# Kernel optimization log

Hardware: AMD Instinct MI355X
Metric: run time of the kernel (lower is better)

The kernel has to match this reference:

```python
import jax, jax.numpy as jnp
import numpy as np

DRUG_DIM, PROT_DIM, HIDDEN_DIM, OUTPUT_DIM = 128, 128, 256, 256


def setup_inputs() -> dict:
    key = jax.random.key(0)
    ks = jax.random.split(key, 7)
    B, n_d, n_p = 8, 64, 1024
    s = lambda d: 1.0 / np.sqrt(d)
    return {
        "X_d": jax.random.normal(ks[0], (B, n_d, DRUG_DIM), dtype=jnp.float32),
        "X_p": jax.random.normal(ks[1], (B, n_p, PROT_DIM), dtype=jnp.float32),
        # nn.Linear(in, out) weights have shape (out, in); we store transposed (in, out)
        "W_d": jax.random.uniform(ks[2], (DRUG_DIM, HIDDEN_DIM), jnp.float32, -s(DRUG_DIM), s(DRUG_DIM)),
        "W_p": jax.random.uniform(ks[3], (PROT_DIM, HIDDEN_DIM), jnp.float32, -s(PROT_DIM), s(PROT_DIM)),
        "W_a": jax.random.uniform(ks[4], (DRUG_DIM, OUTPUT_DIM), jnp.float32, -s(DRUG_DIM), s(DRUG_DIM)),
        "W_b": jax.random.uniform(ks[5], (PROT_DIM, OUTPUT_DIM), jnp.float32, -s(PROT_DIM), s(PROT_DIM)),
        "w_score": jax.random.uniform(ks[6], (HIDDEN_DIM,), jnp.float32, -s(HIDDEN_DIM), s(HIDDEN_DIM)),
    }


def reference(X_d, X_p, W_d, W_p, W_a, W_b, w_score):
    # Projections: (B, n_d, H), (B, n_p, H), (B, n_d, O), (B, n_p, O)
    hd = jnp.einsum("bik,kh->bih", X_d, W_d)
    hp = jnp.einsum("bjk,kh->bjh", X_p, W_p)
    fd = jnp.einsum("bik,ko->bio", X_d, W_a)
    fp = jnp.einsum("bjk,ko->bjo", X_p, W_b)

    # N_ij = tanh(hd_i + hp_j): (B, n_d, n_p, H); scores = N @ w_score
    N = jnp.tanh(hd[:, :, None, :] + hp[:, None, :, :])
    scores = jnp.einsum("bijh,h->bij", N, w_score)
    A = jax.nn.softmax(scores, axis=-1)  # softmax over protein dim

    # f_ij = tanh(fd_i + fp_j): (B, n_d, n_p, O)
    f = jnp.tanh(fd[:, :, None, :] + fp[:, None, :, :])
    X_int = jnp.einsum("bij,bijo->bo", A, f)  # sum over i and j
    return X_int
```

## Files before the change

### kernel.cpp

```cpp
#include <hip/hip_runtime.h>

#define NB   8
#define ND   64
#define NP   1024
#define KDIM 128
#define HID  256
#define OUTD 256
#define CSC  2.885390081777927f

typedef __attribute__((ext_vector_type(8))) short  bf16x8;
typedef __attribute__((ext_vector_type(4))) float  f32x4;


__device__ __forceinline__ ushort f2bf(float f) {
    unsigned u = __float_as_uint(f);
    return (ushort)((u + 0x7FFFu + ((u >> 16) & 1u)) >> 16);
}

__global__ __launch_bounds__(256) void k_cast(
    const float* __restrict__ Xd, const float* __restrict__ Xp,
    const float* __restrict__ Wd, const float* __restrict__ Wa,
    const float* __restrict__ Wp, const float* __restrict__ Wb,
    ushort* __restrict__ Xdbf, ushort* __restrict__ Xpbf,
    ushort* __restrict__ WdT, ushort* __restrict__ WaT,
    ushort* __restrict__ WpT, ushort* __restrict__ WbT) {
    int blk = blockIdx.x, t = threadIdx.x;
    if (blk < 1024) {
        size_t i = ((size_t)blk << 10) + ((size_t)t << 2);
        float4 v = *(const float4*)(Xp + i);
        ushort4 o; o.x = f2bf(v.x); o.y = f2bf(v.y); o.z = f2bf(v.z); o.w = f2bf(v.w);
        *(ushort4*)(Xpbf + i) = o;
    } else if (blk < 1088) {
        size_t i = ((size_t)(blk - 1024) << 10) + ((size_t)t << 2);
        float4 v = *(const float4*)(Xd + i);
        ushort4 o; o.x = f2bf(v.x); o.y = f2bf(v.y); o.z = f2bf(v.z); o.w = f2bf(v.w);
        *(ushort4*)(Xdbf + i) = o;
    } else {
        int r = blk - 1088, mat = r >> 5;
        const float* W = (mat == 0) ? Wd : (mat == 1) ? Wa : (mat == 2) ? Wp : Wb;
        ushort* WT = (mat == 0) ? WdT : (mat == 1) ? WaT : (mat == 2) ? WpT : WbT;
        int o0 = ((r & 31) << 10) + (t << 2);
        int n = o0 >> 7, k0 = o0 & 127;
        ushort4 o;
        o.x = f2bf(W[(k0 + 0) * HID + n]);
        o.y = f2bf(W[(k0 + 1) * HID + n]);
        o.z = f2bf(W[(k0 + 2) * HID + n]);
        o.w = f2bf(W[(k0 + 3) * HID + n]);
        *(ushort4*)(WT + o0) = o;
    }
}

__global__ __launch_bounds__(256) void k_proj_mfma(
    const ushort* __restrict__ Xpbf, const ushort* __restrict__ Xdbf,
    const ushort* __restrict__ WdT, const ushort* __restrict__ WaT,
    const ushort* __restrict__ WpT, const ushort* __restrict__ WbT,
    float* __restrict__ Ehd, float* __restrict__ Efd,
    float* __restrict__ EhpT, float* __restrict__ Efp) {
    int blk = blockIdx.x, t = threadIdx.x;
    const ushort *A, *B;
    float* out; size_t obase; int ostride, am0, bn0;
    if (blk < 512) {
        int mt = blk >> 2, nt = blk & 3;
        A = Xpbf; am0 = mt * 64; B = WbT; bn0 = nt * 64;
        out = Efp; obase = (size_t)am0 * HID + bn0; ostride = HID;
    } else if (blk < 1024) {
        int r = blk - 512, b = r >> 6, rr = r & 63;
        int mt = rr >> 4, nt = rr & 15;
        A = WpT; am0 = mt * 64;
        B = Xpbf + (size_t)b * NP * KDIM; bn0 = nt * 64;
        out = EhpT; obase = ((size_t)(b * 256 + am0)) * NP + bn0; ostride = NP;
    } else if (blk < 1056) {
        int r = blk - 1024; int mt = r >> 2, nt = r & 3;
        A = Xdbf; am0 = mt * 64; B = WdT; bn0 = nt * 64;
        out = Ehd; obase = (size_t)am0 * HID + bn0; ostride = HID;
    } else {
        int r = blk - 1056; int mt = r >> 2, nt = r & 3;
        A = Xdbf; am0 = mt * 64; B = WaT; bn0 = nt * 64;
        out = Efd; obase = (size_t)am0 * HID + bn0; ostride = HID;
    }
    int l = t & 63, w = t >> 6;
    int wm = (w >> 1) << 5, wn = (w & 1) << 5;
    int lr = l & 15, lk = (l >> 4) << 3;
    const ushort* Ab = A + (size_t)(am0 + wm + lr) * KDIM + lk;
    const ushort* Bb = B + (size_t)(bn0 + wn + lr) * KDIM + lk;

    bf16x8 af[2][4], bfr[2][4];
#pragma unroll
    for (int f = 0; f < 2; ++f)
#pragma unroll
        for (int ks = 0; ks < 4; ++ks) {
            af[f][ks]  = *(const bf16x8*)(Ab + (size_t)(f << 4) * KDIM + (ks << 5));
            bfr[f][ks] = *(const bf16x8*)(Bb + (size_t)(f << 4) * KDIM + (ks << 5));
        }

    f32x4 acc[2][2];
#pragma unroll
    for (int mf = 0; mf < 2; ++mf)
#pragma unroll
        for (int nf = 0; nf < 2; ++nf) acc[mf][nf] = (f32x4){0.f, 0.f, 0.f, 0.f};
#pragma unroll
    for (int ks = 0; ks < 4; ++ks)
#pragma unroll
        for (int mf = 0; mf < 2; ++mf)
#pragma unroll
            for (int nf = 0; nf < 2; ++nf)
                acc[mf][nf] = __builtin_amdgcn_mfma_f32_16x16x32_bf16(
                    af[mf][ks], bfr[nf][ks], acc[mf][nf], 0, 0, 0);

#pragma unroll
    for (int mf = 0; mf < 2; ++mf)
#pragma unroll
        for (int nf = 0; nf < 2; ++nf)
#pragma unroll
            for (int r = 0; r < 4; ++r) {
                int m = wm + (mf << 4) + ((l >> 4) << 2) + r;
                int n = wn + (nf << 4) + (l & 15);
                out[obase + (size_t)m * ostride + n] =
                    __builtin_amdgcn_exp2f(acc[mf][nf][r] * CSC);
            }
}

__global__ __launch_bounds__(512) void k_fused(
    const float* __restrict__ Ehd, const float* __restrict__ EhpT,
    const float* __restrict__ Efd, const float* __restrict__ Efp,
    const float* __restrict__ wsc, float* __restrict__ part) {
    int blk = blockIdx.x;
    int b = blk >> 6;
    int t = threadIdx.x;
    __shared__ float4 hs4[64];
    __shared__ float4 w24[64];
    __shared__ float4 a2v[256];
    __shared__ float  red[512];
    if (t < 64) {
        hs4[t] = ((const float4*)(Ehd + ((size_t)blk << 8)))[t];
        float4 wv = ((const float4*)wsc)[t];
        w24[t] = make_float4(-2.f * wv.x, -2.f * wv.y, -2.f * wv.z, -2.f * wv.w);
    }
    __syncthreads();

    const float* pT = EhpT + ((size_t)(b << 8)) * NP + t;
    float acc0 = 0.f, acc1 = 0.f;
    for (int h4 = 0; h4 < 64; ++h4) {
        float4 hv = hs4[h4];
        float4 wv = w24[h4];
        const float* pb = pT + (size_t)(h4 << 2) * NP;
        float p0 = pb[0],        q0 = pb[512];
        float p1 = pb[NP],       q1 = pb[NP + 512];
        float p2 = pb[2 * NP],   q2 = pb[2 * NP + 512];
        float p3 = pb[3 * NP],   q3 = pb[3 * NP + 512];
        acc0 = fmaf(wv.x, __builtin_amdgcn_rcpf(fmaf(hv.x, p0, 1.f)), acc0);
        acc1 = fmaf(wv.x, __builtin_amdgcn_rcpf(fmaf(hv.x, q0, 1.f)), acc1);
        acc0 = fmaf(wv.y, __builtin_amdgcn_rcpf(fmaf(hv.y, p1, 1.f)), acc0);
        acc1 = fmaf(wv.y, __builtin_amdgcn_rcpf(fmaf(hv.y, q1, 1.f)), acc1);
        acc0 = fmaf(wv.z, __builtin_amdgcn_rcpf(fmaf(hv.z, p2, 1.f)), acc0);
        acc1 = fmaf(wv.z, __builtin_amdgcn_rcpf(fmaf(hv.z, q2, 1.f)), acc1);
        acc0 = fmaf(wv.w, __builtin_amdgcn_rcpf(fmaf(hv.w, p3, 1.f)), acc0);
        acc1 = fmaf(wv.w, __builtin_amdgcn_rcpf(fmaf(hv.w, q3, 1.f)), acc1);
    }

    const float L2E = 1.4426950408889634f;
    float e0 = __builtin_amdgcn_exp2f(acc0 * L2E);
    float e1 = __builtin_amdgcn_exp2f(acc1 * L2E);
    float s4 = e0 + e1;
#pragma unroll
    for (int off = 32; off > 0; off >>= 1) s4 += __shfl_xor(s4, off, 64);
    __shared__ float wsum[8];
    if ((t & 63) == 0) wsum[t >> 6] = s4;
    __syncthreads();
    float tot = ((wsum[0] + wsum[1]) + (wsum[2] + wsum[3])) +
                ((wsum[4] + wsum[5]) + (wsum[6] + wsum[7]));
    float sneg = -2.0f * __builtin_amdgcn_rcpf(tot);
    float* a2 = (float*)a2v;
    a2[t]       = e0 * sneg;
    a2[t + 512] = e1 * sneg;
    __syncthreads();

    int o = t & 255, half = t >> 8;
    float fdv = Efd[((size_t)blk << 8) + o];
    const float* fp = Efp + (((size_t)(b * NP + (half << 9))) << 8) + o;
    const float4* ah = a2v + (half << 7);
    float accA = 0.f, accB = 0.f;
    for (int j4 = 0; j4 < 128; ++j4) {
        const float* fj = fp + ((size_t)j4 << 10);
        float f0 = fj[0];
        float f1 = fj[256];
        float f2 = fj[512];
        float f3 = fj[768];
        float4 av = ah[j4];
        accA = fmaf(av.x, __builtin_amdgcn_rcpf(fmaf(fdv, f0, 1.f)), accA);
        accB = fmaf(av.y, __builtin_amdgcn_rcpf(fmaf(fdv, f1, 1.f)), accB);
        accA = fmaf(av.z, __builtin_amdgcn_rcpf(fmaf(fdv, f2, 1.f)), accA);
        accB = fmaf(av.w, __builtin_amdgcn_rcpf(fmaf(fdv, f3, 1.f)), accB);
    }
    red[t] = accA + accB;
    __syncthreads();
    if (t < 256)
        part[((size_t)blk << 8) + t] = red[t] + red[t + 256];
}

__global__ __launch_bounds__(256) void k_reduce(
    const float* __restrict__ part, float* __restrict__ out) {
    int b = blockIdx.x, t = threadIdx.x;
    float s = 64.0f;
#pragma unroll 8
    for (int i = 0; i < 64; ++i)
        s += part[((size_t)(b * 64 + i) << 8) + t];
    out[(b << 8) + t] = s;
}

extern "C" void kernel_launch(void* const* d_in, const int* in_sizes, int n_in,
                              void* d_out, int out_size, void* d_ws, size_t ws_size,
                              hipStream_t stream) {
    const float* Xd  = (const float*)d_in[0];
    const float* Xp  = (const float*)d_in[1];
    const float* Wd  = (const float*)d_in[2];
    const float* Wp  = (const float*)d_in[3];
    const float* Wa  = (const float*)d_in[4];
    const float* Wb  = (const float*)d_in[5];
    const float* wsc = (const float*)d_in[6];
    float* out = (float*)d_out;

    float* ws = (float*)d_ws;
    float* Ehd  = ws;
    float* Efd  = Ehd + NB * ND * HID;
    float* EhpT = Efd + NB * ND * OUTD;
    float* Efp  = EhpT + NB * NP * HID;
    float* stage = Efp + NB * NP * OUTD;
    ushort* Xpbf = (ushort*)stage;
    ushort* Xdbf = Xpbf + NB * NP * KDIM;
    ushort* WdT  = Xdbf + 65536;
    ushort* WaT  = WdT + 32768;
    ushort* WpT  = WaT + 32768;
    ushort* WbT  = WpT + 32768;
    float* part  = stage;

    k_cast     <<<1216, 256, 0, stream>>>(Xd, Xp, Wd, Wa, Wp, Wb,
                                          Xdbf, Xpbf, WdT, WaT, WpT, WbT);
    k_proj_mfma<<<1088, 256, 0, stream>>>(Xpbf, Xdbf, WdT, WaT, WpT, WbT,
                                          Ehd, Efd, EhpT, Efp);
    k_fused    <<<NB * ND, 512, 0, stream>>>(Ehd, EhpT, Efd, Efp, wsc, part);
    k_reduce   <<<NB, 256, 0, stream>>>(part, out);
}
```

Before: 71.74 us.

## Use 1024-thread blocks in fused kernel and interleave batch across blocks

The fused attention kernel now uses 1024 threads per block, one per protein position, instead of 512 threads each handling two. The output-accumulation phase splits the protein dimension into four quarters instead of two. The block-to-(batch,row) mapping is interleaved so that consecutive blocks touch different batches, and the reduce kernel's indexing is changed to match. This is meant to increase thread-level parallelism and spread memory traffic across batches. The cost is fewer registers per thread, less ILP per thread, and a larger final in-block reduction.

```diff
diff --git a/kernel.cpp b/kernel.cpp
--- a/kernel.cpp
+++ b/kernel.cpp
@@ -120,67 +120,63 @@
             }
 }
 
-__global__ __launch_bounds__(512) void k_fused(
+__global__ __launch_bounds__(1024) void k_fused(
     const float* __restrict__ Ehd, const float* __restrict__ EhpT,
     const float* __restrict__ Efd, const float* __restrict__ Efp,
     const float* __restrict__ wsc, float* __restrict__ part) {
     int blk = blockIdx.x;
-    int b = blk >> 6;
+    int b = blk & 7, i = blk >> 3;
+    int row = b * ND + i;
     int t = threadIdx.x;
     __shared__ float4 hs4[64];
     __shared__ float4 w24[64];
     __shared__ float4 a2v[256];
-    __shared__ float  red[512];
+    __shared__ float  red[1024];
+    __shared__ float  wsum[16];
     if (t < 64) {
-        hs4[t] = ((const float4*)(Ehd + ((size_t)blk << 8)))[t];
+        hs4[t] = ((const float4*)(Ehd + ((size_t)row << 8)))[t];
         float4 wv = ((const float4*)wsc)[t];
         w24[t] = make_float4(-2.f * wv.x, -2.f * wv.y, -2.f * wv.z, -2.f * wv.w);
     }
     __syncthreads();
 
     const float* pT = EhpT + ((size_t)(b << 8)) * NP + t;
-    float acc0 = 0.f, acc1 = 0.f;
+    float acc0 = 0.f;
     for (int h4 = 0; h4 < 64; ++h4) {
         float4 hv = hs4[h4];
         float4 wv = w24[h4];
         const float* pb = pT + (size_t)(h4 << 2) * NP;
-        float p0 = pb[0],        q0 = pb[512];
-        float p1 = pb[NP],       q1 = pb[NP + 512];
-        float p2 = pb[2 * NP],   q2 = pb[2 * NP + 512];
-        float p3 = pb[3 * NP],   q3 = pb[3 * NP + 512];
+        float p0 = pb[0];
+        float p1 = pb[NP];
+        float p2 = pb[2 * NP];
+        float p3 = pb[3 * NP];
         acc0 = fmaf(wv.x, __builtin_amdgcn_rcpf(fmaf(hv.x, p0, 1.f)), acc0);
-        acc1 = fmaf(wv.x, __builtin_amdgcn_rcpf(fmaf(hv.x, q0, 1.f)), acc1);
         acc0 = fmaf(wv.y, __builtin_amdgcn_rcpf(fmaf(hv.y, p1, 1.f)), acc0);
-        acc1 = fmaf(wv.y, __builtin_amdgcn_rcpf(fmaf(hv.y, q1, 1.f)), acc1);
         acc0 = fmaf(wv.z, __builtin_amdgcn_rcpf(fmaf(hv.z, p2, 1.f)), acc0);
-        acc1 = fmaf(wv.z, __builtin_amdgcn_rcpf(fmaf(hv.z, q2, 1.f)), acc1);
         acc0 = fmaf(wv.w, __builtin_amdgcn_rcpf(fmaf(hv.w, p3, 1.f)), acc0);
-        acc1 = fmaf(wv.w, __builtin_amdgcn_rcpf(fmaf(hv.w, q3, 1.f)), acc1);
     }
 
     const float L2E = 1.4426950408889634f;
     float e0 = __builtin_amdgcn_exp2f(acc0 * L2E);
-    float e1 = __builtin_amdgcn_exp2f(acc1 * L2E);
-    float s4 = e0 + e1;
+    float s4 = e0;
 #pragma unroll
     for (int off = 32; off > 0; off >>= 1) s4 += __shfl_xor(s4, off, 64);
-    __shared__ float wsum[8];
     if ((t & 63) == 0) wsum[t >> 6] = s4;
     __syncthreads();
-    float tot = ((wsum[0] + wsum[1]) + (wsum[2] + wsum[3])) +
-                ((wsum[4] + wsum[5]) + (wsum[6] + wsum[7]));
+    float tot = (((wsum[0] + wsum[1]) + (wsum[2] + wsum[3])) +
+                 ((wsum[4] + wsum[5]) + (wsum[6] + wsum[7]))) +
+                (((wsum[8] + wsum[9]) + (wsum[10] + wsum[11])) +
+                 ((wsum[12] + wsum[13]) + (wsum[14] + wsum[15])));
     float sneg = -2.0f * __builtin_amdgcn_rcpf(tot);
-    float* a2 = (float*)a2v;
-    a2[t]       = e0 * sneg;
-    a2[t + 512] = e1 * sneg;
-    __syncthreads();
-
-    int o = t & 255, half = t >> 8;
-    float fdv = Efd[((size_t)blk << 8) + o];
-    const float* fp = Efp + (((size_t)(b * NP + (half << 9))) << 8) + o;
-    const float4* ah = a2v + (half << 7);
+    ((float*)a2v)[t] = e0 * sneg;
+    __syncthreads();
+
+    int o = t & 255, q = t >> 8;
+    float fdv = Efd[((size_t)row << 8) + o];
+    const float* fp = Efp + (((size_t)(b * NP + (q << 8))) << 8) + o;
+    const float4* ah = a2v + (q << 6);
     float accA = 0.f, accB = 0.f;
-    for (int j4 = 0; j4 < 128; ++j4) {
+    for (int j4 = 0; j4 < 64; ++j4) {
         const float* fj = fp + ((size_t)j4 << 10);
         float f0 = fj[0];
         float f1 = fj[256];
@@ -195,7 +191,8 @@
     red[t] = accA + accB;
     __syncthreads();
     if (t < 256)
-        part[((size_t)blk << 8) + t] = red[t] + red[t + 256];
+        part[((size_t)blk << 8) + t] =
+            (red[t] + red[t + 256]) + (red[t + 512] + red[t + 768]);
 }
 
 __global__ __launch_bounds__(256) void k_reduce(
@@ -204,7 +201,7 @@
     float s = 64.0f;
 #pragma unroll 8
     for (int i = 0; i < 64; ++i)
-        s += part[((size_t)(b * 64 + i) << 8) + t];
+        s += part[((size_t)(i * 8 + b) << 8) + t];
     out[(b << 8) + t] = s;
 }
 
@@ -238,6 +235,6 @@
                                           Xdbf, Xpbf, WdT, WaT, WpT, WbT);
     k_proj_mfma<<<1088, 256, 0, stream>>>(Xpbf, Xdbf, WdT, WaT, WpT, WbT,
                                           Ehd, Efd, EhpT, Efp);
-    k_fused    <<<NB * ND, 512, 0, stream>>>(Ehd, EhpT, Efd, Efp, wsc, part);
+    k_fused    <<<NB * ND, 1024, 0, stream>>>(Ehd, EhpT, Efd, Efp, wsc, part);
     k_reduce   <<<NB, 256, 0, stream>>>(part, out);
 }
```

Measured after the change: 74.38 us. 3.7% more time.
